# Optimization experiments

Measured on AMD Instinct MI355X. Metric: run time of the kernel, lower is better.

Reference implementation:

```python
import jax, jax.numpy as jnp
import numpy as np

EMBED = 256
NUM_DEPTH = 128
NUM_CAMS = 1


def _bilinear_sample(img, x, y):
    # img: [H, W, E]; x, y: [L] pixel coords (align_corners=False, zero padding)
    H, W, _ = img.shape
    x0f = jnp.floor(x); y0f = jnp.floor(y)
    ix0 = x0f.astype(jnp.int32); iy0 = y0f.astype(jnp.int32)
    ix1 = ix0 + 1; iy1 = iy0 + 1
    wx1 = x - x0f; wx0 = 1.0 - wx1
    wy1 = y - y0f; wy0 = 1.0 - wy1

    def g(iy, ix):
        valid = (ix >= 0) & (ix < W) & (iy >= 0) & (iy < H)
        v = img[jnp.clip(iy, 0, H - 1), jnp.clip(ix, 0, W - 1)]  # [L, E]
        return jnp.where(valid[:, None], v, jnp.zeros((), img.dtype))

    return (g(iy0, ix0) * (wy0 * wx0)[:, None] + g(iy0, ix1) * (wy0 * wx1)[:, None]
            + g(iy1, ix0) * (wy1 * wx0)[:, None] + g(iy1, ix1) * (wy1 * wx1)[:, None])


def setup_inputs() -> dict:
    rng = jax.random.key(0)
    ks = jax.random.split(rng, 7)
    H = W = 64
    nv = H * W           # num_value == num_query (forced by output*key broadcast)
    bsv = 1
    return {
        "query": jax.random.normal(ks[0], (bsv, nv, EMBED), jnp.float32),
        "key": jax.random.normal(ks[1], (NUM_CAMS, nv, bsv, EMBED), jnp.float32),
        "value": jax.random.normal(ks[2], (NUM_CAMS, nv, bsv, EMBED), jnp.float32),
        "identity": jax.random.normal(ks[3], (bsv, nv, NUM_DEPTH), jnp.float32),
        "ref_3d": jax.random.uniform(ks[4], (bsv * NUM_CAMS, nv * NUM_DEPTH, 2), jnp.float32),
        "spatial_shapes": jnp.array([[H, W]], jnp.int32),
        "W_attn": jax.random.normal(ks[5], (NUM_CAMS * NUM_DEPTH, EMBED), jnp.float32) * 0.02,
        "b_attn": jax.random.normal(ks[6], (NUM_CAMS * NUM_DEPTH,), jnp.float32) * 0.02,
    }


def reference(query, key, value, identity, ref_3d, spatial_shapes, W_attn, b_attn):
    bsv, num_query, _ = query.shape
    num_cams, num_value, bs, _ = key.shape
    H = int(spatial_shapes[0, 0]); W = int(spatial_shapes[0, 1])

    # key/value rearrange (value flipped over cams dim, a no-op for num_cams=1)
    key_r = jnp.transpose(key, (2, 0, 1, 3)).reshape(bsv, num_value, EMBED)
    val_r = jnp.transpose(value[::-1], (2, 0, 1, 3)).reshape(bsv * num_cams, num_value, EMBED)

    # attention weights: Linear -> softmax over (levels*points)=1 axis (== ones)
    aw = query @ W_attn.T + b_attn                               # [bsv, nq, cams*depth]
    aw = aw.reshape(bsv, num_query, num_cams, NUM_DEPTH, 1, 1)    # heads=1, lv*pt=1
    aw = jax.nn.softmax(aw, axis=-1)
    aw = jnp.transpose(aw.reshape(bsv, num_query, num_cams, NUM_DEPTH, 1, 1, 1),
                       (0, 2, 1, 3, 4, 5, 6))
    aw = aw.reshape(bsv * num_cams, num_query * NUM_DEPTH)        # [B, L]

    # deformable bilinear sampling (single level/head/point)
    grids = 2.0 * ref_3d - 1.0                                   # grid_sample convention
    px = ((grids[..., 0] + 1.0) * W - 1.0) / 2.0                  # [B, L]
    py = ((grids[..., 1] + 1.0) * H - 1.0) / 2.0
    imgs = val_r.reshape(bsv * num_cams, H, W, EMBED)
    sampled = jax.vmap(_bilinear_sample)(imgs, px, py)            # [B, L, E]

    out = sampled * aw[:, :, None]                                # weighted gather
    out = out.reshape(bsv, num_cams, num_query, NUM_DEPTH, EMBED).mean(axis=1)

    # elementwise dot with key features, scaled
    out = jnp.sum(out * key_r[:, :, None, :], axis=-1) / jnp.sqrt(jnp.float32(EMBED))
    return out + identity                                         # [bsv, nq, num_depth]
```

## Files before the change

### kernel.cpp

```cpp
#include <hip/hip_runtime.h>

#define EMBED 256
#define NUM_DEPTH 128
#define CT_STRIDE 136

typedef __attribute__((ext_vector_type(8))) short bf16x8;
typedef __attribute__((ext_vector_type(4))) float f32x4;

__device__ __forceinline__ unsigned short f2b(float f) {
    union { float f; unsigned u; } c; c.f = f;
    unsigned u = c.u;
    u += 0x7fffu + ((u >> 16) & 1u);
    return (unsigned short)(u >> 16);
}
__device__ __forceinline__ float b2f(unsigned short h) {
    union { unsigned u; float f; } c; c.u = ((unsigned)h) << 16;
    return c.f;
}

__global__ __launch_bounds__(256) void cvt_kernel(
    const float4* __restrict__ key, const float4* __restrict__ val,
    ushort4* __restrict__ kb, ushort4* __restrict__ vb, int n4)
{
    int i = blockIdx.x * blockDim.x + threadIdx.x;
    if (i >= n4) return;
    float4 a = key[i];
    float4 b = val[i];
    kb[i] = make_ushort4(f2b(a.x), f2b(a.y), f2b(a.z), f2b(a.w));
    vb[i] = make_ushort4(f2b(b.x), f2b(b.y), f2b(b.z), f2b(b.w));
}

__global__ __launch_bounds__(256) void gemm_nt_bf16(
    const unsigned short* __restrict__ A,
    const unsigned short* __restrict__ B,
    unsigned short* __restrict__ D,
    int N)
{
    __shared__ __align__(16) unsigned short Ct[128 * CT_STRIDE];
    unsigned short* As = Ct;
    unsigned short* Bs = Ct + 128 * 32;

    const int m0 = blockIdx.y * 128;
    const int n0 = blockIdx.x * 128;
    const int tid  = threadIdx.x;
    const int lane = tid & 63;
    const int wave = tid >> 6;
    const int wm = (wave & 1) * 64;
    const int wn = (wave >> 1) * 64;

    f32x4 acc[4][4] = {};

    const int srow = lane >> 2;
    const int scol = (lane & 3) * 8;
    const int k8 = (lane >> 4) * 8;
    const int fm = lane & 15;

    for (int kt = 0; kt < EMBED; kt += 32) {
        #pragma unroll
        for (int t = 0; t < 2; ++t) {
            const int c = wave * 2 + t;
            const int row = c * 16 + srow;
            const unsigned short* ga = A + (size_t)(m0 + row) * EMBED + kt + scol;
            const unsigned short* gb = B + (size_t)(n0 + row) * EMBED + kt + scol;
            __builtin_amdgcn_global_load_lds(
                (const __attribute__((address_space(1))) void*)ga,
                (__attribute__((address_space(3))) void*)(As + c * 512), 16, 0, 0);
            __builtin_amdgcn_global_load_lds(
                (const __attribute__((address_space(1))) void*)gb,
                (__attribute__((address_space(3))) void*)(Bs + c * 512), 16, 0, 0);
        }
        __syncthreads();

        bf16x8 af[4], bfr[4];
        #pragma unroll
        for (int i = 0; i < 4; ++i) {
            af[i]  = *(const bf16x8*)(As + (wm + i * 16 + fm) * 32 + k8);
            bfr[i] = *(const bf16x8*)(Bs + (wn + i * 16 + fm) * 32 + k8);
        }
        #pragma unroll
        for (int i = 0; i < 4; ++i)
            #pragma unroll
            for (int j = 0; j < 4; ++j)
                acc[i][j] = __builtin_amdgcn_mfma_f32_16x16x32_bf16(af[i], bfr[j], acc[i][j], 0, 0, 0);
        __syncthreads();
    }

    const int col = lane & 15;
    const int rbase = (lane >> 4) * 4;
    #pragma unroll
    for (int i = 0; i < 4; ++i)
        #pragma unroll
        for (int j = 0; j < 4; ++j) {
            const int rr = wm + i * 16 + rbase;
            const int cc = wn + j * 16 + col;
            #pragma unroll
            for (int r = 0; r < 4; ++r)
                Ct[(rr + r) * CT_STRIDE + cc] = f2b(acc[i][j][r]);
        }
    __syncthreads();

    #pragma unroll
    for (int it = 0; it < 8; ++it) {
        const int r  = it * 16 + (tid >> 4);
        const int c8 = (tid & 15) * 8;
        const int4 v = *(const int4*)(Ct + r * CT_STRIDE + c8);
        *(int4*)(D + (size_t)(m0 + r) * N + n0 + c8) = v;
    }
}

__global__ __launch_bounds__(256) void gather_kernel(
    const unsigned short* __restrict__ D,
    const float* __restrict__ identity,
    const float* __restrict__ ref3d,
    const int*   __restrict__ spatial,
    float* __restrict__ out, int nv)
{
    __shared__ unsigned short Ds[2 * 4096];

    const int q0 = blockIdx.x * 2;
    const int tid = threadIdx.x;

    const int4* src = (const int4*)(D + (size_t)q0 * nv);
    int4* dst = (int4*)Ds;
    const int nchunk = (2 * nv) / 8;
    for (int i = tid; i < nchunk; i += 256) dst[i] = src[i];
    __syncthreads();

    const int Hs = spatial[0], Ws = spatial[1];
    const int l = q0 * NUM_DEPTH + tid;
    const int qi = tid >> 7;

    const float2 r2 = reinterpret_cast<const float2*>(ref3d)[l];
    const float px = r2.x * (float)Ws - 0.5f;
    const float py = r2.y * (float)Hs - 0.5f;
    const float x0f = floorf(px), y0f = floorf(py);
    const int ix0 = (int)x0f, iy0 = (int)y0f;
    const int ix1 = ix0 + 1,  iy1 = iy0 + 1;
    const float wx1 = px - x0f, wx0 = 1.0f - wx1;
    const float wy1 = py - y0f, wy0 = 1.0f - wy1;
    const bool vx0 = (ix0 >= 0) & (ix0 < Ws);
    const bool vx1 = (ix1 >= 0) & (ix1 < Ws);

    const unsigned short* row = Ds + qi * nv;
    float acc = 0.f;
    if (iy0 >= 0 && iy0 < Hs) {
        if (vx0) acc = fmaf(wy0 * wx0, b2f(row[iy0 * Ws + ix0]), acc);
        if (vx1) acc = fmaf(wy0 * wx1, b2f(row[iy0 * Ws + ix1]), acc);
    }
    if (iy1 >= 0 && iy1 < Hs) {
        if (vx0) acc = fmaf(wy1 * wx0, b2f(row[iy1 * Ws + ix0]), acc);
        if (vx1) acc = fmaf(wy1 * wx1, b2f(row[iy1 * Ws + ix1]), acc);
    }
    out[l] = fmaf(acc, 0.0625f, identity[l]);
}

__global__ __launch_bounds__(256) void uv_direct_kernel(
    const float* __restrict__ key, const float* __restrict__ value,
    const float* __restrict__ identity, const float* __restrict__ ref3d,
    const int* __restrict__ spatial, float* __restrict__ out)
{
    const int q = blockIdx.x;
    const int tid = threadIdx.x;
    const int lane = tid & 63;
    const int wave = tid >> 6;
    const int H = spatial[0], W = spatial[1];
    const int row4 = EMBED / 4;
    const float4 k4 = reinterpret_cast<const float4*>(key + (size_t)q * EMBED)[lane];
    const float4* __restrict__ v4 = reinterpret_cast<const float4*>(value);
    for (int d = wave; d < NUM_DEPTH; d += 4) {
        const int l = q * NUM_DEPTH + d;
        const float rx = ref3d[2 * l], ry = ref3d[2 * l + 1];
        const float px = rx * (float)W - 0.5f, py = ry * (float)H - 0.5f;
        const float x0f = floorf(px), y0f = floorf(py);
        const int ix0 = (int)x0f, iy0 = (int)y0f, ix1 = ix0 + 1, iy1 = iy0 + 1;
        const float wx1 = px - x0f, wx0 = 1.f - wx1, wy1 = py - y0f, wy0 = 1.f - wy1;
        float4 acc = make_float4(0.f, 0.f, 0.f, 0.f);
        #define TAP(IY, IX, WGT) \
            if ((IY) >= 0 && (IY) < H && (IX) >= 0 && (IX) < W) { \
                const float w_ = (WGT); \
                const float4 t = v4[(size_t)((IY) * W + (IX)) * row4 + lane]; \
                acc.x = fmaf(w_, t.x, acc.x); acc.y = fmaf(w_, t.y, acc.y); \
                acc.z = fmaf(w_, t.z, acc.z); acc.w = fmaf(w_, t.w, acc.w); }
        TAP(iy0, ix0, wy0 * wx0) TAP(iy0, ix1, wy0 * wx1)
        TAP(iy1, ix0, wy1 * wx0) TAP(iy1, ix1, wy1 * wx1)
        #undef TAP
        float partial = acc.x * k4.x + acc.y * k4.y + acc.z * k4.z + acc.w * k4.w;
        #pragma unroll
        for (int off = 32; off > 0; off >>= 1) partial += __shfl_xor(partial, off, 64);
        if (lane == 0) out[l] = fmaf(partial, 0.0625f, identity[l]);
    }
}

extern "C" void kernel_launch(void* const* d_in, const int* in_sizes, int n_in,
                              void* d_out, int out_size, void* d_ws, size_t ws_size,
                              hipStream_t stream) {
    const float* key      = (const float*)d_in[1];
    const float* value    = (const float*)d_in[2];
    const float* identity = (const float*)d_in[3];
    const float* ref3d    = (const float*)d_in[4];
    const int*   spatial  = (const int*)d_in[5];
    float* out = (float*)d_out;

    const int nq = in_sizes[3] / NUM_DEPTH;
    const int nv = in_sizes[1] / EMBED;

    const size_t d_bytes  = (size_t)nq * nv * sizeof(unsigned short);
    const size_t kb_bytes = (size_t)nq * EMBED * sizeof(unsigned short);
    const size_t vb_bytes = (size_t)nv * EMBED * sizeof(unsigned short);
    const size_t need = d_bytes + kb_bytes + vb_bytes;

    if (ws_size < need || (nq % 128) || (nv % 128) || nv > 4096 || (nq % 2)) {
        uv_direct_kernel<<<nq, 256, 0, stream>>>(key, value, identity, ref3d, spatial, out);
        return;
    }

    unsigned short* D  = (unsigned short*)d_ws;
    unsigned short* kb = (unsigned short*)((char*)d_ws + d_bytes);
    unsigned short* vb = (unsigned short*)((char*)d_ws + d_bytes + kb_bytes);

    const int n4 = nq * EMBED / 4;
    cvt_kernel<<<(n4 + 255) / 256, 256, 0, stream>>>(
        (const float4*)key, (const float4*)value, (ushort4*)kb, (ushort4*)vb, n4);

    dim3 grid(nv / 128, nq / 128);
    gemm_nt_bf16<<<grid, 256, 0, stream>>>(kb, vb, D, nv);

    gather_kernel<<<nq / 2, 256, 0, stream>>>(D, identity, ref3d, spatial, out, nv);
}
```

Measured before the change: 99.00 us.

## Double GEMM K-tile to 64 and remap LDS layout to avoid bank conflicts

The bf16 NT GEMM now loads a 64-wide K slice per iteration, halving the number of barrier-separated loop trips. The LDS tile layout is reorganized so each lane's 16-byte fragment sits contiguously by k-group and row (kg*128 + r16*8). The global-to-LDS load mapping changes to match, so fragment reads hit consecutive addresses and avoid the strided pattern of the old row*32 layout. The cost is more shared memory per tile, still within the existing Ct buffer, and more fragment registers live per iteration.

```diff
diff --git a/kernel.cpp b/kernel.cpp
--- a/kernel.cpp
+++ b/kernel.cpp
@@ -38,7 +38,7 @@
 {
     __shared__ __align__(16) unsigned short Ct[128 * CT_STRIDE];
     unsigned short* As = Ct;
-    unsigned short* Bs = Ct + 128 * 32;
+    unsigned short* Bs = Ct + 8192;
 
     const int m0 = blockIdx.y * 128;
     const int n0 = blockIdx.x * 128;
@@ -50,38 +50,44 @@
 
     f32x4 acc[4][4] = {};
 
-    const int srow = lane >> 2;
-    const int scol = (lane & 3) * 8;
-    const int k8 = (lane >> 4) * 8;
-    const int fm = lane & 15;
-
-    for (int kt = 0; kt < EMBED; kt += 32) {
+    const int r16 = lane & 15;
+    const int kg  = lane >> 4;
+
+    for (int kt = 0; kt < EMBED; kt += 64) {
         #pragma unroll
         for (int t = 0; t < 2; ++t) {
             const int c = wave * 2 + t;
-            const int row = c * 16 + srow;
-            const unsigned short* ga = A + (size_t)(m0 + row) * EMBED + kt + scol;
-            const unsigned short* gb = B + (size_t)(n0 + row) * EMBED + kt + scol;
-            __builtin_amdgcn_global_load_lds(
-                (const __attribute__((address_space(1))) void*)ga,
-                (__attribute__((address_space(3))) void*)(As + c * 512), 16, 0, 0);
-            __builtin_amdgcn_global_load_lds(
-                (const __attribute__((address_space(1))) void*)gb,
-                (__attribute__((address_space(3))) void*)(Bs + c * 512), 16, 0, 0);
+            const int grow = c * 16 + r16;
+            #pragma unroll
+            for (int h = 0; h < 2; ++h) {
+                const unsigned short* ga = A + (size_t)(m0 + grow) * EMBED + kt + h * 32 + kg * 8;
+                const unsigned short* gb = B + (size_t)(n0 + grow) * EMBED + kt + h * 32 + kg * 8;
+                __builtin_amdgcn_global_load_lds(
+                    (const __attribute__((address_space(1))) void*)ga,
+                    (__attribute__((address_space(3))) void*)(As + c * 1024 + h * 512), 16, 0, 0);
+                __builtin_amdgcn_global_load_lds(
+                    (const __attribute__((address_space(1))) void*)gb,
+                    (__attribute__((address_space(3))) void*)(Bs + c * 1024 + h * 512), 16, 0, 0);
+            }
         }
         __syncthreads();
 
-        bf16x8 af[4], bfr[4];
-        #pragma unroll
-        for (int i = 0; i < 4; ++i) {
-            af[i]  = *(const bf16x8*)(As + (wm + i * 16 + fm) * 32 + k8);
-            bfr[i] = *(const bf16x8*)(Bs + (wn + i * 16 + fm) * 32 + k8);
+        #pragma unroll
+        for (int kk = 0; kk < 2; ++kk) {
+            bf16x8 af[4], bfr[4];
+            #pragma unroll
+            for (int i = 0; i < 4; ++i) {
+                const int ca = (wm + i * 16) >> 4;
+                const int cb = (wn + i * 16) >> 4;
+                af[i]  = *(const bf16x8*)(As + ca * 1024 + kk * 512 + kg * 128 + r16 * 8);
+                bfr[i] = *(const bf16x8*)(Bs + cb * 1024 + kk * 512 + kg * 128 + r16 * 8);
+            }
+            #pragma unroll
+            for (int i = 0; i < 4; ++i)
+                #pragma unroll
+                for (int j = 0; j < 4; ++j)
+                    acc[i][j] = __builtin_amdgcn_mfma_f32_16x16x32_bf16(af[i], bfr[j], acc[i][j], 0, 0, 0);
         }
-        #pragma unroll
-        for (int i = 0; i < 4; ++i)
-            #pragma unroll
-            for (int j = 0; j < 4; ++j)
-                acc[i][j] = __builtin_amdgcn_mfma_f32_16x16x32_bf16(af[i], bfr[j], acc[i][j], 0, 0, 0);
         __syncthreads();
     }
 
```

Result: slower. 106.6 us (+7.7%).

## Fuse bilinear gather into GEMM epilogue with atomic scatter, drop D buffer

Applied to the files above, without the earlier changes.

Removes the bf16 score matrix D and the separate gather kernel. Each GEMM tile now samples its bilinear taps straight from the LDS tile and atomically adds partial results into the output. The output is pre-filled with identity inside the conversion kernel. This avoids writing and re-reading the nq×nv intermediate (32 MB) and one launch. In exchange, every tile has to scan all 128×128 ref points of its query block, and atomics are added. It also assumes W divides 128, and tile rows line up with image rows.

```diff
diff --git a/kernel.cpp b/kernel.cpp
--- a/kernel.cpp
+++ b/kernel.cpp
@@ -18,30 +18,35 @@
     return c.f;
 }
 
-__global__ __launch_bounds__(256) void cvt_kernel(
+__global__ __launch_bounds__(256) void cvt_init_kernel(
     const float4* __restrict__ key, const float4* __restrict__ val,
-    ushort4* __restrict__ kb, ushort4* __restrict__ vb, int n4)
+    ushort4* __restrict__ kb, ushort4* __restrict__ vb, int n4,
+    const float4* __restrict__ id4, float4* __restrict__ out4, int nid4)
 {
     int i = blockIdx.x * blockDim.x + threadIdx.x;
-    if (i >= n4) return;
-    float4 a = key[i];
-    float4 b = val[i];
-    kb[i] = make_ushort4(f2b(a.x), f2b(a.y), f2b(a.z), f2b(a.w));
-    vb[i] = make_ushort4(f2b(b.x), f2b(b.y), f2b(b.z), f2b(b.w));
-}
-
-__global__ __launch_bounds__(256) void gemm_nt_bf16(
+    if (i < n4) {
+        float4 a = key[i];
+        float4 b = val[i];
+        kb[i] = make_ushort4(f2b(a.x), f2b(a.y), f2b(a.z), f2b(a.w));
+        vb[i] = make_ushort4(f2b(b.x), f2b(b.y), f2b(b.z), f2b(b.w));
+    }
+    if (i < nid4) out4[i] = id4[i];
+}
+
+__global__ __launch_bounds__(256) void gemm_scatter_kernel(
     const unsigned short* __restrict__ A,
     const unsigned short* __restrict__ B,
-    unsigned short* __restrict__ D,
-    int N)
+    const float* __restrict__ ref3d,
+    const int*   __restrict__ spatial,
+    float* __restrict__ out)
 {
     __shared__ __align__(16) unsigned short Ct[128 * CT_STRIDE];
     unsigned short* As = Ct;
     unsigned short* Bs = Ct + 128 * 32;
 
     const int m0 = blockIdx.y * 128;
-    const int n0 = blockIdx.x * 128;
+    const int jt = blockIdx.x;
+    const int n0 = jt * 128;
     const int tid  = threadIdx.x;
     const int lane = tid & 63;
     const int wave = tid >> 6;
@@ -99,59 +104,41 @@
         }
     __syncthreads();
 
-    #pragma unroll
-    for (int it = 0; it < 8; ++it) {
-        const int r  = it * 16 + (tid >> 4);
-        const int c8 = (tid & 15) * 8;
-        const int4 v = *(const int4*)(Ct + r * CT_STRIDE + c8);
-        *(int4*)(D + (size_t)(m0 + r) * N + n0 + c8) = v;
-    }
-}
-
-__global__ __launch_bounds__(256) void gather_kernel(
-    const unsigned short* __restrict__ D,
-    const float* __restrict__ identity,
-    const float* __restrict__ ref3d,
-    const int*   __restrict__ spatial,
-    float* __restrict__ out, int nv)
-{
-    __shared__ unsigned short Ds[2 * 4096];
-
-    const int q0 = blockIdx.x * 2;
-    const int tid = threadIdx.x;
-
-    const int4* src = (const int4*)(D + (size_t)q0 * nv);
-    int4* dst = (int4*)Ds;
-    const int nchunk = (2 * nv) / 8;
-    for (int i = tid; i < nchunk; i += 256) dst[i] = src[i];
-    __syncthreads();
-
-    const int Hs = spatial[0], Ws = spatial[1];
-    const int l = q0 * NUM_DEPTH + tid;
-    const int qi = tid >> 7;
-
-    const float2 r2 = reinterpret_cast<const float2*>(ref3d)[l];
-    const float px = r2.x * (float)Ws - 0.5f;
-    const float py = r2.y * (float)Hs - 0.5f;
-    const float x0f = floorf(px), y0f = floorf(py);
-    const int ix0 = (int)x0f, iy0 = (int)y0f;
-    const int ix1 = ix0 + 1,  iy1 = iy0 + 1;
-    const float wx1 = px - x0f, wx0 = 1.0f - wx1;
-    const float wy1 = py - y0f, wy0 = 1.0f - wy1;
-    const bool vx0 = (ix0 >= 0) & (ix0 < Ws);
-    const bool vx1 = (ix1 >= 0) & (ix1 < Ws);
-
-    const unsigned short* row = Ds + qi * nv;
-    float acc = 0.f;
-    if (iy0 >= 0 && iy0 < Hs) {
-        if (vx0) acc = fmaf(wy0 * wx0, b2f(row[iy0 * Ws + ix0]), acc);
-        if (vx1) acc = fmaf(wy0 * wx1, b2f(row[iy0 * Ws + ix1]), acc);
-    }
-    if (iy1 >= 0 && iy1 < Hs) {
-        if (vx0) acc = fmaf(wy1 * wx0, b2f(row[iy1 * Ws + ix0]), acc);
-        if (vx1) acc = fmaf(wy1 * wx1, b2f(row[iy1 * Ws + ix1]), acc);
-    }
-    out[l] = fmaf(acc, 0.0625f, identity[l]);
+    const int H = spatial[0], W = spatial[1];
+    const int Rt = 128 / W;
+    const int iy_lo = Rt * jt;
+    const float2* __restrict__ r3 = (const float2*)ref3d;
+
+    for (int e = tid; e < 128 * NUM_DEPTH; e += 256) {
+        const int ql = e >> 7;
+        const int l = (m0 + ql) * NUM_DEPTH + (e & 127);
+        const float2 r2 = r3[l];
+        const float px = r2.x * (float)W - 0.5f;
+        const float py = r2.y * (float)H - 0.5f;
+        const float x0f = floorf(px), y0f = floorf(py);
+        const int iy0 = (int)y0f;
+        if (iy0 + 1 < iy_lo || iy0 >= iy_lo + Rt) continue;
+
+        const int ix0 = (int)x0f;
+        const float wx1 = px - x0f, wx0 = 1.0f - wx1;
+        const float wy1 = py - y0f, wy0 = 1.0f - wy1;
+        const bool vx0 = (ix0 >= 0) & (ix0 < W);
+        const bool vx1 = (ix0 + 1 >= 0) & (ix0 + 1 < W);
+
+        float accv = 0.f;
+        bool hit = false;
+        #pragma unroll
+        for (int ky = 0; ky < 2; ++ky) {
+            const int iy = iy0 + ky;
+            if (iy < iy_lo || iy >= iy_lo + Rt) continue;
+            const float wy = ky ? wy1 : wy0;
+            const int pb = ql * CT_STRIDE + (iy - iy_lo) * W;
+            if (vx0) { accv = fmaf(wy * wx0, b2f(Ct[pb + ix0]), accv); hit = true; }
+            if (vx1) { accv = fmaf(wy * wx1, b2f(Ct[pb + ix0 + 1]), accv); hit = true; }
+        }
+        if (hit)
+            atomicAdd(&out[l], accv * 0.0625f);
+    }
 }
 
 __global__ __launch_bounds__(256) void uv_direct_kernel(
@@ -204,26 +191,24 @@
     const int nq = in_sizes[3] / NUM_DEPTH;
     const int nv = in_sizes[1] / EMBED;
 
-    const size_t d_bytes  = (size_t)nq * nv * sizeof(unsigned short);
     const size_t kb_bytes = (size_t)nq * EMBED * sizeof(unsigned short);
     const size_t vb_bytes = (size_t)nv * EMBED * sizeof(unsigned short);
-    const size_t need = d_bytes + kb_bytes + vb_bytes;
-
-    if (ws_size < need || (nq % 128) || (nv % 128) || nv > 4096 || (nq % 2)) {
+    const size_t need = kb_bytes + vb_bytes;
+
+    if (ws_size < need || (nq % 128) || (nv % 128)) {
         uv_direct_kernel<<<nq, 256, 0, stream>>>(key, value, identity, ref3d, spatial, out);
         return;
     }
 
-    unsigned short* D  = (unsigned short*)d_ws;
-    unsigned short* kb = (unsigned short*)((char*)d_ws + d_bytes);
-    unsigned short* vb = (unsigned short*)((char*)d_ws + d_bytes + kb_bytes);
-
-    const int n4 = nq * EMBED / 4;
-    cvt_kernel<<<(n4 + 255) / 256, 256, 0, stream>>>(
-        (const float4*)key, (const float4*)value, (ushort4*)kb, (ushort4*)vb, n4);
+    unsigned short* kb = (unsigned short*)d_ws;
+    unsigned short* vb = (unsigned short*)((char*)d_ws + kb_bytes);
+
+    const int n4   = nq * EMBED / 4;
+    const int nid4 = nq * NUM_DEPTH / 4;
+    cvt_init_kernel<<<(n4 + 255) / 256, 256, 0, stream>>>(
+        (const float4*)key, (const float4*)value, (ushort4*)kb, (ushort4*)vb, n4,
+        (const float4*)identity, (float4*)out, nid4);
 
     dim3 grid(nv / 128, nq / 128);
-    gemm_nt_bf16<<<grid, 256, 0, stream>>>(kb, vb, D, nv);
-
-    gather_kernel<<<nq / 2, 256, 0, stream>>>(D, identity, ref3d, spatial, out, nv);
-}
+    gemm_scatter_kernel<<<grid, 256, 0, stream>>>(kb, vb, ref3d, spatial, out);
+}
```

Measured after the change: 152.5 us. 1.54x slower.
